# Optimization experiments

Hardware: AMD Instinct MI355X
Metric: run time of the kernel (lower is better)

## Reference

```python
import jax, jax.numpy as jnp
import numpy as np
import math

PS = 8          # patch_size
OUT_C = 16      # out_channels
D_MODEL = 64
P_STATE = 32
BANDLIMIT = 1.0
STEP_SCALE = 1.0  # dt1 reference rate


def _ln(x, g, b, eps=1e-5):
    mu = jnp.mean(x, -1, keepdims=True)
    var = jnp.mean((x - mu) ** 2, -1, keepdims=True)
    return (x - mu) * jax.lax.rsqrt(var + eps) * g + b


def _forward(x, W_embed, b_embed, g1, beta1, Lambda_re, Lambda_im, B_re, B_im,
             C_re, C_im, D, log_step, g2, beta2, W_enc, W_dec, g3, beta3, W_out, b_out):
    b, t, h, w = x.shape
    hp, wp = h // PS, w // PS
    n = hp * wp
    # patchify: [b,t,h,w] -> [b,t,n,ps*ps]
    xp = x.reshape(b, t, hp, PS, wp, PS).transpose(0, 1, 2, 4, 3, 5).reshape(b, t, n, PS * PS)
    xe = xp @ W_embed.T + b_embed                              # [b,t,n,d]
    u = xe.transpose(0, 2, 1, 3).reshape(b * n, t, D_MODEL)    # [(b n), t, d]

    # ---- S5Block: pre-norm -> diagonal SSM -> gelu + residual -> GEGLU FFN ----
    fx = _ln(u, g1, beta1)
    Lam = Lambda_re + 1j * Lambda_im                           # [P] complex eigenvalues
    step = STEP_SCALE * jnp.exp(log_step)                      # [P]
    Lbar = jnp.exp(Lam * step)                                 # ZOH: A_bar
    Bbar = ((Lbar - 1.0) / Lam)[:, None] * (B_re + 1j * B_im)  # ZOH: B_bar [P,d]
    # bandlimit mask on C (freqs = step*|Im(Lambda)|/(2pi) < bandlimit/2)
    freqs = step * jnp.abs(Lambda_im) / (2.0 * math.pi)
    mask = (freqs < BANDLIMIT * 0.5).astype(C_re.dtype)
    Cc = (C_re + 1j * C_im) * mask[None, :]                    # [d,P]

    Bu = jnp.einsum('ntd,pd->ntp', fx.astype(jnp.complex64), Bbar)   # [(bn),t,P]
    A = jnp.broadcast_to(Lbar.astype(jnp.complex64), (1, t, P_STATE))

    def comb(e1, e2):
        a1, b1 = e1
        a2, b2 = e2
        return a1 * a2, a2 * b1 + b2

    _, xs = jax.lax.associative_scan(comb, (A, Bu), axis=1)    # x_k = A*x_{k-1} + Bu_k (x_0 = 0)
    ys = jnp.einsum('ntp,dp->ntd', xs, Cc).real + fx * D       # y = Re(C x) + D u
    xb = jax.nn.gelu(ys, approximate=False) + fx

    fx2 = _ln(xb, g2, beta2)
    enc = fx2 @ W_enc.T                                        # [(bn),t,2d]
    a, gate = jnp.split(enc, 2, axis=-1)
    xb = (a * jax.nn.gelu(gate, approximate=False)) @ W_dec.T + fx2

    # ---- take last timestep, project, unpatchify ----
    x_last = xb[:, -1, :]                                      # [(bn), d]
    proj = _ln(x_last, g3, beta3) @ W_out.T + b_out            # [(bn), C*ps*ps]
    y = proj.reshape(b, hp, wp, OUT_C, PS, PS).transpose(0, 3, 1, 4, 2, 5).reshape(b, OUT_C, h, w)
    return y


def setup_inputs() -> dict:
    key = jax.random.key(0)
    ks = jax.random.split(key, 12)
    d, P, pp = D_MODEL, P_STATE, PS * PS
    return dict(
        x=jax.random.normal(ks[0], (8, 15, 480, 640), jnp.float32),
        W_embed=jax.random.normal(ks[1], (d, pp), jnp.float32) / math.sqrt(pp),
        b_embed=jnp.zeros((d,), jnp.float32),
        g1=jnp.ones((d,), jnp.float32), beta1=jnp.zeros((d,), jnp.float32),
        Lambda_re=-0.5 * jnp.ones((P,), jnp.float32),
        Lambda_im=math.pi * (1.0 + jnp.arange(P, dtype=jnp.float32)),
        B_re=jax.random.normal(ks[2], (P, d), jnp.float32) / math.sqrt(d),
        B_im=jax.random.normal(ks[3], (P, d), jnp.float32) / math.sqrt(d),
        C_re=jax.random.normal(ks[4], (d, P), jnp.float32) / math.sqrt(P),
        C_im=jax.random.normal(ks[5], (d, P), jnp.float32) / math.sqrt(P),
        D=jax.random.normal(ks[6], (d,), jnp.float32),
        log_step=jax.random.uniform(ks[7], (P,), jnp.float32, math.log(1e-3), math.log(1e-1)),
        g2=jnp.ones((d,), jnp.float32), beta2=jnp.zeros((d,), jnp.float32),
        W_enc=jax.random.normal(ks[8], (2 * d, d), jnp.float32) / math.sqrt(d),
        W_dec=jax.random.normal(ks[9], (d, d), jnp.float32) / math.sqrt(d),
        g3=jnp.ones((d,), jnp.float32), beta3=jnp.zeros((d,), jnp.float32),
        W_out=jax.random.normal(ks[10], (OUT_C * pp, d), jnp.float32) / math.sqrt(d),
        b_out=jnp.zeros((OUT_C * pp,), jnp.float32),
    )


def reference(x, W_embed, b_embed, g1, beta1, Lambda_re, Lambda_im, B_re, B_im,
              C_re, C_im, D, log_step, g2, beta2, W_enc, W_dec, g3, beta3, W_out, b_out):
    return _forward(x, W_embed, b_embed, g1, beta1, Lambda_re, Lambda_im, B_re, B_im,
                    C_re, C_im, D, log_step, g2, beta2, W_enc, W_dec, g3, beta3, W_out, b_out)
```

## Files before the change

kernel.cpp:

```cpp
#include <hip/hip_runtime.h>
#include <math.h>


typedef __attribute__((ext_vector_type(8))) short short8;
typedef __attribute__((ext_vector_type(4))) float f32x4;

#define MFMA16(a, b, c) __builtin_amdgcn_mfma_f32_16x16x32_bf16((a), (b), (c), 0, 0, 0)

__device__ __forceinline__ short f2bf(float f) {
  union { float f; unsigned u; } v; v.f = f;
  unsigned r = (v.u + 0x7fffu + ((v.u >> 16) & 1u)) >> 16;
  return (short)r;
}
__device__ __forceinline__ float geluf(float x) {
  return 0.5f * x * (1.0f + erff(x * 0.70710678118654752f));
}
__device__ __forceinline__ short8 packfrag(const f32x4& a, const f32x4& b) {
  short8 o;
  o[0] = f2bf(a[0]); o[1] = f2bf(a[1]); o[2] = f2bf(a[2]); o[3] = f2bf(a[3]);
  o[4] = f2bf(b[0]); o[5] = f2bf(b[1]); o[6] = f2bf(b[2]); o[7] = f2bf(b[3]);
  return o;
}
__device__ __forceinline__ int ecmap(int i, int m) {
  return (i >> 1) * 32 + (m >> 2) * 8 + (i & 1) * 4 + (m & 3);
}
__device__ __forceinline__ void bbar_factors(const float* Lre, const float* Lim,
                                             const float* lstep, int p,
                                             float& fre, float& fim) {
  float st = expf(lstep[p]);
  float lr = Lre[p], li = Lim[p];
  float er = expf(lr * st);
  float lbr = er * cosf(li * st), lbi = er * sinf(li * st);
  float u = lbr - 1.0f, v = lbi;
  float den = lr * lr + li * li;
  fre = (u * lr + v * li) / den;
  fim = (v * lr - u * li) / den;
}

__global__ __launch_bounds__(256) void k0_prep(
    const float* __restrict__ W_embed, const float* __restrict__ g1,
    const float* __restrict__ be1, const float* __restrict__ Lre,
    const float* __restrict__ Lim, const float* __restrict__ Bre,
    const float* __restrict__ Bim, const float* __restrict__ Cre,
    const float* __restrict__ Cim, const float* __restrict__ lstep,
    const float* __restrict__ W_enc, const float* __restrict__ W_dec,
    const float* __restrict__ W_out, short* __restrict__ wimg,
    float* __restrict__ bu0) {
  const int bid = blockIdx.x;
  if (bid == 44) {
    int q = threadIdx.x;
    if (q < 64) {
      int c = q >> 5, p = q & 31;
      float fre, fim; bbar_factors(Lre, Lim, lstep, p, fre, fim);
      float s = 0.f;
      for (int d = 0; d < 64; ++d) {
        float br = Bre[p * 64 + d], bi = Bim[p * 64 + d];
        float val = c ? (fre * bi + fim * br) : (fre * br - fim * bi);
        s += be1[d] * val;
      }
      bu0[q] = s;
    }
    return;
  }
  const int w = threadIdx.x >> 6, lane = threadIdx.x & 63;
  const int m = lane & 15, qd = lane >> 4;
  const int f = bid * 4 + w;
  short v[8];
  if (f < 8) {
    int i = f >> 1, kt = f & 1, chan = ecmap(i, m), k0 = kt * 32 + qd * 8;
#pragma unroll
    for (int j = 0; j < 8; ++j) v[j] = f2bf(W_embed[chan * 64 + k0 + j]);
  } else if (f < 16) {
    int fi = f - 8, i = fi >> 1, kt = fi & 1;
    int comp = i & 1, p = (i >> 1) * 16 + m, d0 = kt * 32 + qd * 8;
    float fre, fim; bbar_factors(Lre, Lim, lstep, p, fre, fim);
#pragma unroll
    for (int j = 0; j < 8; ++j) {
      int d = d0 + j;
      float br = Bre[p * 64 + d], bi = Bim[p * 64 + d];
      float val = comp ? (fre * bi + fim * br) : (fre * br - fim * bi);
      v[j] = f2bf(g1[d] * val);
    }
  } else if (f < 24) {
    int fi = f - 16, i = fi >> 1, kt = fi & 1, chan = ecmap(i, m);
#pragma unroll
    for (int j = 0; j < 8; ++j) {
      int comp = j >> 2, p = kt * 16 + qd * 4 + (j & 3);
      float stp = expf(lstep[p]);
      float fr = stp * fabsf(Lim[p]) * (1.0f / 6.28318530717958648f);
      float msk = (fr < 0.5f) ? 1.f : 0.f;
      float val = comp ? -Cim[chan * 32 + p] * msk : Cre[chan * 32 + p] * msk;
      v[j] = f2bf(val);
    }
  } else if (f < 40) {
    int fi = f - 24, i = fi >> 1, kt = fi & 1;
    int row = (i < 4) ? ecmap(i, m) : 64 + ecmap(i - 4, m);
#pragma unroll
    for (int j = 0; j < 8; ++j) v[j] = f2bf(W_enc[row * 64 + kt * 32 + qd * 8 + j]);
  } else if (f < 48) {
    int fi = f - 40, i = fi >> 1, kt = fi & 1, row = ecmap(i, m);
#pragma unroll
    for (int j = 0; j < 8; ++j) v[j] = f2bf(W_dec[row * 64 + kt * 32 + qd * 8 + j]);
  } else {
    int fi = f - 48, i = fi >> 1, kt = fi & 1, row = i * 16 + m;
#pragma unroll
    for (int j = 0; j < 8; ++j) v[j] = f2bf(W_out[row * 64 + kt * 32 + qd * 8 + j]);
  }
  short8 sv;
#pragma unroll
  for (int j = 0; j < 8; ++j) sv[j] = v[j];
  *(short8*)&wimg[(f * 64 + lane) * 8] = sv;
}

__global__ __launch_bounds__(320) void k1_fused(
    const float* __restrict__ x, const short* __restrict__ wimg_g,
    const float* __restrict__ bu0_g, const float* __restrict__ Lre,
    const float* __restrict__ Lim, const float* __restrict__ lstep,
    const float* __restrict__ g1, const float* __restrict__ be1,
    const float* __restrict__ bemb, const float* __restrict__ Dv,
    const float* __restrict__ g2, const float* __restrict__ be2,
    const float* __restrict__ g3, const float* __restrict__ be3,
    const float* __restrict__ b_out, float* __restrict__ y) {
  __shared__ __align__(16) char smem[57344];
#define WF(id) (*(const short8*)(smem + (id) * 1024 + lane * 16))

  const int tid = threadIdx.x;
  const int wv = tid >> 6, lane = tid & 63;
  const int s = lane & 15, qd = lane >> 4;

  int cb[4];
  f32x4 bec[4], bu0c[4];
#pragma unroll
  for (int nt = 0; nt < 4; ++nt) {
    cb[nt] = (nt >> 1) * 32 + qd * 8 + (nt & 1) * 4;
    bec[nt] = *(const f32x4*)(bemb + cb[nt]);
    bu0c[nt] = *(const f32x4*)(bu0_g + (nt & 1) * 32 + (nt >> 1) * 16 + qd * 4);
  }
  f32x4 lbr[2], lbi[2];
#pragma unroll
  for (int k = 0; k < 2; ++k)
#pragma unroll
    for (int r = 0; r < 4; ++r) {
      int p = k * 16 + qd * 4 + r;
      float st = expf(lstep[p]);
      float er = expf(Lre[p] * st);
      lbr[k][r] = er * cosf(Lim[p] * st);
      lbi[k][r] = er * sinf(Lim[p] * st);
    }

  const int b_i = blockIdx.x / 60;
  const int ph = blockIdx.x % 60;
  const int tb0 = ((b_i * 15) * 480 + ph * 8) * 640;
  const int sbase = blockIdx.x * 80 + wv * 16;
  int rb[4];
#pragma unroll
  for (int kt = 0; kt < 2; ++kt)
#pragma unroll
    for (int h = 0; h < 2; ++h)
      rb[kt * 2 + h] = (kt * 4 + qd) * 2560 + (wv * 16 + s) * 32 + h * 16;

#define STAGE(bufofs, tt)                                                     \
  {                                                                           \
    const float* gsrc = x + tb0 + (tt) * 307200 + wv * 1024;                  \
    char* lb = smem + (bufofs) + wv * 4096;                                   \
    _Pragma("unroll") for (int j = 0; j < 4; ++j)                             \
        __builtin_amdgcn_global_load_lds(                                     \
            (const __attribute__((address_space(1))) void*)(gsrc + j * 256 +  \
                                                            lane * 4),        \
            (__attribute__((address_space(3))) void*)(lb + j * 1024),         \
            16, 0, 0);                                                        \
  }

  STAGE(16384, 0);
  STAGE(36864, 1);
  {
    float4* wdst = (float4*)smem;
    const float4* wsrc = (const float4*)wimg_g;
    for (int i = tid; i < 1024; i += 320) wdst[i] = wsrc[i];
  }
  asm volatile("s_waitcnt vmcnt(0) lgkmcnt(0)" ::: "memory");
  __builtin_amdgcn_s_barrier();

  const f32x4 zf = {0.f, 0.f, 0.f, 0.f};
  f32x4 state[4] = {zf, zf, zf, zf};
  f32x4 xh[4];

  for (int t = 0; t < 15; ++t) {
    const char* bufr = smem + 16384 + (t & 1) * 20480;
    f32x4 vcur[4];
#pragma unroll
    for (int q = 0; q < 4; ++q) vcur[q] = *(const f32x4*)(bufr + rb[q]);
    asm volatile("s_waitcnt lgkmcnt(0)" ::: "memory");
    __builtin_amdgcn_s_barrier();
    if (t < 13) STAGE(16384 + (t & 1) * 20480, t + 2);

    short8 pa0 = packfrag(vcur[0], vcur[1]);
    short8 pa1 = packfrag(vcur[2], vcur[3]);
    f32x4 c1[4];
#pragma unroll
    for (int i = 0; i < 4; ++i) {
      f32x4 acc = MFMA16(WF(i * 2), pa0, zf);
      acc = MFMA16(WF(i * 2 + 1), pa1, acc);
      c1[i] = acc + bec[i];
    }
    float sm = 0.f, sq = 0.f;
#pragma unroll
    for (int nt = 0; nt < 4; ++nt)
#pragma unroll
      for (int i = 0; i < 4; ++i) { sm += c1[nt][i]; sq += c1[nt][i] * c1[nt][i]; }
    sm += __shfl_xor(sm, 16); sq += __shfl_xor(sq, 16);
    sm += __shfl_xor(sm, 32); sq += __shfl_xor(sq, 32);
    float mean = sm * 0.015625f;
    float rstd = rsqrtf(sq * 0.015625f - mean * mean + 1e-5f);
#pragma unroll
    for (int nt = 0; nt < 4; ++nt) xh[nt] = (c1[nt] - mean) * rstd;
    short8 xa0 = packfrag(xh[0], xh[1]);
    short8 xa1 = packfrag(xh[2], xh[3]);
#pragma unroll
    for (int k = 0; k < 2; ++k) {
      f32x4 re = state[2 * k], im = state[2 * k + 1];
      state[2 * k]     = lbr[k] * re - lbi[k] * im + bu0c[2 * k];
      state[2 * k + 1] = lbr[k] * im + lbi[k] * re + bu0c[2 * k + 1];
    }
#pragma unroll
    for (int i = 0; i < 4; ++i) {
      state[i] = MFMA16(WF(8 + i * 2), xa0, state[i]);
      state[i] = MFMA16(WF(8 + i * 2 + 1), xa1, state[i]);
    }

    if (t < 14) {
      if (t < 13) asm volatile("s_waitcnt vmcnt(4)" ::: "memory");
      else        asm volatile("s_waitcnt vmcnt(0)" ::: "memory");
      __builtin_amdgcn_s_barrier();
    }
  }
#undef STAGE

  __syncthreads();
  {
    float4* dst = (float4*)(smem + 16384);
    const float4* src = (const float4*)(wimg_g + 16 * 512);
    for (int i = tid; i < 2048; i += 320) dst[i] = src[i];
  }
  __syncthreads();

  f32x4 g1c[4], b1c[4], Dc[4], g2c[4], b2c[4];
#pragma unroll
  for (int nt = 0; nt < 4; ++nt) {
    g1c[nt] = *(const f32x4*)(g1 + cb[nt]);
    b1c[nt] = *(const f32x4*)(be1 + cb[nt]);
    Dc[nt] = *(const f32x4*)(Dv + cb[nt]);
    g2c[nt] = *(const f32x4*)(g2 + cb[nt]);
    b2c[nt] = *(const f32x4*)(be2 + cb[nt]);
  }
  f32x4 fxl[4];
#pragma unroll
  for (int nt = 0; nt < 4; ++nt) fxl[nt] = xh[nt] * g1c[nt] + b1c[nt];

  short8 xsa0 = packfrag(state[0], state[1]);
  short8 xsa1 = packfrag(state[2], state[3]);
  f32x4 xbv[4];
#pragma unroll
  for (int i = 0; i < 4; ++i) {
    f32x4 acc = fxl[i] * Dc[i];
    acc = MFMA16(WF(16 + i * 2), xsa0, acc);
    acc = MFMA16(WF(16 + i * 2 + 1), xsa1, acc);
#pragma unroll
    for (int r = 0; r < 4; ++r) xbv[i][r] = geluf(acc[r]) + fxl[i][r];
  }
  float sm2 = 0.f, sq2 = 0.f;
#pragma unroll
  for (int nt = 0; nt < 4; ++nt)
#pragma unroll
    for (int i = 0; i < 4; ++i) { sm2 += xbv[nt][i]; sq2 += xbv[nt][i] * xbv[nt][i]; }
  sm2 += __shfl_xor(sm2, 16); sq2 += __shfl_xor(sq2, 16);
  sm2 += __shfl_xor(sm2, 32); sq2 += __shfl_xor(sq2, 32);
  float mean2 = sm2 * 0.015625f;
  float rstd2 = rsqrtf(sq2 * 0.015625f - mean2 * mean2 + 1e-5f);
  f32x4 fx2[4];
#pragma unroll
  for (int nt = 0; nt < 4; ++nt)
    fx2[nt] = (xbv[nt] - mean2) * rstd2 * g2c[nt] + b2c[nt];

  short8 fa0 = packfrag(fx2[0], fx2[1]);
  short8 fa1 = packfrag(fx2[2], fx2[3]);
  f32x4 e[8];
#pragma unroll
  for (int i = 0; i < 8; ++i) {
    f32x4 acc = MFMA16(WF(24 + i * 2), fa0, zf);
    e[i] = MFMA16(WF(24 + i * 2 + 1), fa1, acc);
  }
  f32x4 hv[4];
#pragma unroll
  for (int nt = 0; nt < 4; ++nt)
#pragma unroll
    for (int i = 0; i < 4; ++i) hv[nt][i] = e[nt][i] * geluf(e[nt + 4][i]);

  short8 ha0 = packfrag(hv[0], hv[1]);
  short8 ha1 = packfrag(hv[2], hv[3]);
  f32x4 xo[4];
#pragma unroll
  for (int i = 0; i < 4; ++i) {
    f32x4 acc = fx2[i];
    acc = MFMA16(WF(40 + i * 2), ha0, acc);
    xo[i] = MFMA16(WF(40 + i * 2 + 1), ha1, acc);
  }

  float sm3 = 0.f, sq3 = 0.f;
#pragma unroll
  for (int nt = 0; nt < 4; ++nt)
#pragma unroll
    for (int i = 0; i < 4; ++i) { sm3 += xo[nt][i]; sq3 += xo[nt][i] * xo[nt][i]; }
  sm3 += __shfl_xor(sm3, 16); sq3 += __shfl_xor(sq3, 16);
  sm3 += __shfl_xor(sm3, 32); sq3 += __shfl_xor(sq3, 32);
  float mean3 = sm3 * 0.015625f;
  float rstd3 = rsqrtf(sq3 * 0.015625f - mean3 * mean3 + 1e-5f);
  f32x4 z[4];
#pragma unroll
  for (int nt = 0; nt < 4; ++nt) {
    f32x4 g3c = *(const f32x4*)(g3 + cb[nt]);
    f32x4 b3c = *(const f32x4*)(be3 + cb[nt]);
    z[nt] = (xo[nt] - mean3) * rstd3 * g3c + b3c;
  }
  short8 za = packfrag(z[0], z[1]);
  short8 zb = packfrag(z[2], z[3]);

  const int seq = sbase + s;
  const int bi2 = seq / 4800, prr = seq % 4800;
  const int phh = prr / 80, pww = prr % 80;
  const int obase = (bi2 * 16 * 480 + phh * 8) * 640 + pww * 8;
  const short* wob = wimg_g + 48 * 512;

#pragma unroll 4
  for (int ntg = 0; ntg < 64; ++ntg) {
    short8 a0 = *(const short8*)&wob[(ntg * 2 + 0) * 512 + lane * 8];
    short8 a1 = *(const short8*)&wob[(ntg * 2 + 1) * 512 + lane * 8];
    int o0 = ntg * 16 + qd * 4;
    f32x4 acc = *(const f32x4*)(b_out + o0);
    acc = MFMA16(a0, za, acc);
    acc = MFMA16(a1, zb, acc);
    int c = o0 >> 6, pi = (o0 >> 3) & 7, pj = o0 & 7;
    *(f32x4*)&y[obase + c * 307200 + pi * 640 + pj] = acc;
  }
#undef WF
}

extern "C" void kernel_launch(void* const* d_in, const int* in_sizes, int n_in,
                              void* d_out, int out_size, void* d_ws, size_t ws_size,
                              hipStream_t stream) {
  const float* x       = (const float*)d_in[0];
  const float* W_embed = (const float*)d_in[1];
  const float* b_embed = (const float*)d_in[2];
  const float* g1      = (const float*)d_in[3];
  const float* beta1   = (const float*)d_in[4];
  const float* Lre     = (const float*)d_in[5];
  const float* Lim     = (const float*)d_in[6];
  const float* Bre     = (const float*)d_in[7];
  const float* Bim     = (const float*)d_in[8];
  const float* Cre     = (const float*)d_in[9];
  const float* Cim     = (const float*)d_in[10];
  const float* Dv      = (const float*)d_in[11];
  const float* lstep   = (const float*)d_in[12];
  const float* g2      = (const float*)d_in[13];
  const float* beta2   = (const float*)d_in[14];
  const float* W_enc   = (const float*)d_in[15];
  const float* W_dec   = (const float*)d_in[16];
  const float* g3      = (const float*)d_in[17];
  const float* beta3   = (const float*)d_in[18];
  const float* W_out   = (const float*)d_in[19];
  const float* b_out   = (const float*)d_in[20];
  float* y = (float*)d_out;

  short* wimg = (short*)d_ws;
  float* bu0 = (float*)((char*)d_ws + 176 * 1024);

  k0_prep<<<dim3(45), dim3(256), 0, stream>>>(W_embed, g1, beta1, Lre, Lim,
                                              Bre, Bim, Cre, Cim, lstep,
                                              W_enc, W_dec, W_out, wimg, bu0);
  k1_fused<<<dim3(480), dim3(320), 0, stream>>>(x, wimg, bu0, Lre, Lim, lstep,
                                                g1, beta1, b_embed, Dv, g2,
                                                beta2, g3, beta3, b_out, y);
}
```

Measured before the change: 338.6 us.

## Replace LDS-staged input pipeline with direct register prefetch and drop shared memory

Removes the shared-memory double-buffered global_load_lds staging of x and the LDS copies of weight fragments. Each wave now loads its input rows straight into registers with a three-deep rotating prefetch, keeps the first 16 weight fragments in registers, and reads the rest from global or cache. Blocks shrink from 5 to 4 waves and the grid grows from 480 to 600. This drops barriers and LDS traffic and allows higher occupancy, at the cost of more registers and less coalesced global loads.

```diff
diff --git a/kernel.cpp b/kernel.cpp
--- a/kernel.cpp
+++ b/kernel.cpp
@@ -112,7 +112,53 @@
   *(short8*)&wimg[(f * 64 + lane) * 8] = sv;
 }
 
-__global__ __launch_bounds__(320) void k1_fused(
+
+#define LOADX(X, T)                                                           \
+  {                                                                           \
+    const float* rp_ = xbase + (T) * 307200;                                  \
+    X[0] = *(const f32x4*)rp_;                                                \
+    X[1] = *(const f32x4*)(rp_ + 4);                                          \
+    X[2] = *(const f32x4*)(rp_ + 2560);                                       \
+    X[3] = *(const f32x4*)(rp_ + 2564);                                       \
+  }
+
+#define BODY(X, T)                                                            \
+  {                                                                           \
+    short8 pa0 = packfrag(X[0], X[1]);                                        \
+    short8 pa1 = packfrag(X[2], X[3]);                                        \
+    if ((T) + 3 < 15) LOADX(X, (T) + 3);                                      \
+    f32x4 c1[4];                                                              \
+    _Pragma("unroll") for (int i = 0; i < 4; ++i) {                           \
+      f32x4 acc = MFMA16(we[i * 2], pa0, zf);                                 \
+      acc = MFMA16(we[i * 2 + 1], pa1, acc);                                  \
+      c1[i] = acc + bec[i];                                                   \
+    }                                                                         \
+    float sm = 0.f, sq = 0.f;                                                 \
+    _Pragma("unroll") for (int nt = 0; nt < 4; ++nt)                          \
+        _Pragma("unroll") for (int i = 0; i < 4; ++i) {                       \
+      sm += c1[nt][i];                                                        \
+      sq += c1[nt][i] * c1[nt][i];                                            \
+    }                                                                         \
+    sm += __shfl_xor(sm, 16); sq += __shfl_xor(sq, 16);                       \
+    sm += __shfl_xor(sm, 32); sq += __shfl_xor(sq, 32);                       \
+    float mean = sm * 0.015625f;                                              \
+    float rstd = rsqrtf(sq * 0.015625f - mean * mean + 1e-5f);                \
+    _Pragma("unroll") for (int nt = 0; nt < 4; ++nt)                          \
+        xh[nt] = (c1[nt] - mean) * rstd;                                      \
+    short8 xa0 = packfrag(xh[0], xh[1]);                                      \
+    short8 xa1 = packfrag(xh[2], xh[3]);                                      \
+    _Pragma("unroll") for (int k = 0; k < 2; ++k) {                           \
+      f32x4 re = state[2 * k], im = state[2 * k + 1];                         \
+      state[2 * k]     = lbr[k] * re - lbi[k] * im + bu0c[2 * k];             \
+      state[2 * k + 1] = lbr[k] * im + lbi[k] * re + bu0c[2 * k + 1];         \
+    }                                                                         \
+    _Pragma("unroll") for (int i = 0; i < 4; ++i) {                           \
+      state[i] = MFMA16(we[8 + i * 2], xa0, state[i]);                        \
+      state[i] = MFMA16(we[8 + i * 2 + 1], xa1, state[i]);                    \
+    }                                                                         \
+  }
+
+__global__ __launch_bounds__(256) void k1_fused(
     const float* __restrict__ x, const short* __restrict__ wimg_g,
     const float* __restrict__ bu0_g, const float* __restrict__ Lre,
     const float* __restrict__ Lim, const float* __restrict__ lstep,
@@ -121,12 +167,15 @@
     const float* __restrict__ g2, const float* __restrict__ be2,
     const float* __restrict__ g3, const float* __restrict__ be3,
     const float* __restrict__ b_out, float* __restrict__ y) {
-  __shared__ __align__(16) char smem[57344];
-#define WF(id) (*(const short8*)(smem + (id) * 1024 + lane * 16))
+#define GW(id) (*(const short8*)&wimg_g[(id) * 512 + lane * 8])
 
   const int tid = threadIdx.x;
   const int wv = tid >> 6, lane = tid & 63;
   const int s = lane & 15, qd = lane >> 4;
+
+  short8 we[16];
+#pragma unroll
+  for (int i = 0; i < 16; ++i) we[i] = GW(i);
 
   int cb[4];
   f32x4 bec[4], bu0c[4];
@@ -148,101 +197,28 @@
       lbi[k][r] = er * sinf(Lim[p] * st);
     }
 
-  const int b_i = blockIdx.x / 60;
-  const int ph = blockIdx.x % 60;
-  const int tb0 = ((b_i * 15) * 480 + ph * 8) * 640;
-  const int sbase = blockIdx.x * 80 + wv * 16;
-  int rb[4];
-#pragma unroll
-  for (int kt = 0; kt < 2; ++kt)
-#pragma unroll
-    for (int h = 0; h < 2; ++h)
-      rb[kt * 2 + h] = (kt * 4 + qd) * 2560 + (wv * 16 + s) * 32 + h * 16;
-
-#define STAGE(bufofs, tt)                                                     \
-  {                                                                           \
-    const float* gsrc = x + tb0 + (tt) * 307200 + wv * 1024;                  \
-    char* lb = smem + (bufofs) + wv * 4096;                                   \
-    _Pragma("unroll") for (int j = 0; j < 4; ++j)                             \
-        __builtin_amdgcn_global_load_lds(                                     \
-            (const __attribute__((address_space(1))) void*)(gsrc + j * 256 +  \
-                                                            lane * 4),        \
-            (__attribute__((address_space(3))) void*)(lb + j * 1024),         \
-            16, 0, 0);                                                        \
-  }
-
-  STAGE(16384, 0);
-  STAGE(36864, 1);
-  {
-    float4* wdst = (float4*)smem;
-    const float4* wsrc = (const float4*)wimg_g;
-    for (int i = tid; i < 1024; i += 320) wdst[i] = wsrc[i];
-  }
-  asm volatile("s_waitcnt vmcnt(0) lgkmcnt(0)" ::: "memory");
-  __builtin_amdgcn_s_barrier();
+  const int sbase = (blockIdx.x * 4 + wv) * 16;
+  const int b_i = sbase / 4800;
+  const int pr = sbase % 4800;
+  const int ph = pr / 80;
+  const int pw0 = pr % 80;
+  const float* xbase = x + ((b_i * 15) * 480 + ph * 8 + qd) * 640 + (pw0 + s) * 8;
 
   const f32x4 zf = {0.f, 0.f, 0.f, 0.f};
   f32x4 state[4] = {zf, zf, zf, zf};
   f32x4 xh[4];
 
-  for (int t = 0; t < 15; ++t) {
-    const char* bufr = smem + 16384 + (t & 1) * 20480;
-    f32x4 vcur[4];
-#pragma unroll
-    for (int q = 0; q < 4; ++q) vcur[q] = *(const f32x4*)(bufr + rb[q]);
-    asm volatile("s_waitcnt lgkmcnt(0)" ::: "memory");
-    __builtin_amdgcn_s_barrier();
-    if (t < 13) STAGE(16384 + (t & 1) * 20480, t + 2);
-
-    short8 pa0 = packfrag(vcur[0], vcur[1]);
-    short8 pa1 = packfrag(vcur[2], vcur[3]);
-    f32x4 c1[4];
-#pragma unroll
-    for (int i = 0; i < 4; ++i) {
-      f32x4 acc = MFMA16(WF(i * 2), pa0, zf);
-      acc = MFMA16(WF(i * 2 + 1), pa1, acc);
-      c1[i] = acc + bec[i];
-    }
-    float sm = 0.f, sq = 0.f;
-#pragma unroll
-    for (int nt = 0; nt < 4; ++nt)
-#pragma unroll
-      for (int i = 0; i < 4; ++i) { sm += c1[nt][i]; sq += c1[nt][i] * c1[nt][i]; }
-    sm += __shfl_xor(sm, 16); sq += __shfl_xor(sq, 16);
-    sm += __shfl_xor(sm, 32); sq += __shfl_xor(sq, 32);
-    float mean = sm * 0.015625f;
-    float rstd = rsqrtf(sq * 0.015625f - mean * mean + 1e-5f);
-#pragma unroll
-    for (int nt = 0; nt < 4; ++nt) xh[nt] = (c1[nt] - mean) * rstd;
-    short8 xa0 = packfrag(xh[0], xh[1]);
-    short8 xa1 = packfrag(xh[2], xh[3]);
-#pragma unroll
-    for (int k = 0; k < 2; ++k) {
-      f32x4 re = state[2 * k], im = state[2 * k + 1];
-      state[2 * k]     = lbr[k] * re - lbi[k] * im + bu0c[2 * k];
-      state[2 * k + 1] = lbr[k] * im + lbi[k] * re + bu0c[2 * k + 1];
-    }
-#pragma unroll
-    for (int i = 0; i < 4; ++i) {
-      state[i] = MFMA16(WF(8 + i * 2), xa0, state[i]);
-      state[i] = MFMA16(WF(8 + i * 2 + 1), xa1, state[i]);
-    }
-
-    if (t < 14) {
-      if (t < 13) asm volatile("s_waitcnt vmcnt(4)" ::: "memory");
-      else        asm volatile("s_waitcnt vmcnt(0)" ::: "memory");
-      __builtin_amdgcn_s_barrier();
-    }
-  }
-#undef STAGE
-
-  __syncthreads();
-  {
-    float4* dst = (float4*)(smem + 16384);
-    const float4* src = (const float4*)(wimg_g + 16 * 512);
-    for (int i = tid; i < 2048; i += 320) dst[i] = src[i];
-  }
-  __syncthreads();
+  f32x4 xsA[4], xsB[4], xsC[4];
+  LOADX(xsA, 0);
+  LOADX(xsB, 1);
+  LOADX(xsC, 2);
+
+  for (int tt = 0; tt < 5; ++tt) {
+    const int t0 = tt * 3;
+    BODY(xsA, t0 + 0);
+    BODY(xsB, t0 + 1);
+    BODY(xsC, t0 + 2);
+  }
 
   f32x4 g1c[4], b1c[4], Dc[4], g2c[4], b2c[4];
 #pragma unroll
@@ -263,8 +239,8 @@
 #pragma unroll
   for (int i = 0; i < 4; ++i) {
     f32x4 acc = fxl[i] * Dc[i];
-    acc = MFMA16(WF(16 + i * 2), xsa0, acc);
-    acc = MFMA16(WF(16 + i * 2 + 1), xsa1, acc);
+    acc = MFMA16(GW(16 + i * 2), xsa0, acc);
+    acc = MFMA16(GW(16 + i * 2 + 1), xsa1, acc);
 #pragma unroll
     for (int r = 0; r < 4; ++r) xbv[i][r] = geluf(acc[r]) + fxl[i][r];
   }
@@ -287,8 +263,8 @@
   f32x4 e[8];
 #pragma unroll
   for (int i = 0; i < 8; ++i) {
-    f32x4 acc = MFMA16(WF(24 + i * 2), fa0, zf);
-    e[i] = MFMA16(WF(24 + i * 2 + 1), fa1, acc);
+    f32x4 acc = MFMA16(GW(24 + i * 2), fa0, zf);
+    e[i] = MFMA16(GW(24 + i * 2 + 1), fa1, acc);
   }
   f32x4 hv[4];
 #pragma unroll
@@ -302,8 +278,8 @@
 #pragma unroll
   for (int i = 0; i < 4; ++i) {
     f32x4 acc = fx2[i];
-    acc = MFMA16(WF(40 + i * 2), ha0, acc);
-    xo[i] = MFMA16(WF(40 + i * 2 + 1), ha1, acc);
+    acc = MFMA16(GW(40 + i * 2), ha0, acc);
+    xo[i] = MFMA16(GW(40 + i * 2 + 1), ha1, acc);
   }
 
   float sm3 = 0.f, sq3 = 0.f;
@@ -342,7 +318,7 @@
     int c = o0 >> 6, pi = (o0 >> 3) & 7, pj = o0 & 7;
     *(f32x4*)&y[obase + c * 307200 + pi * 640 + pj] = acc;
   }
-#undef WF
+#undef GW
 }
 
 extern "C" void kernel_launch(void* const* d_in, const int* in_sizes, int n_in,
@@ -377,7 +353,7 @@
   k0_prep<<<dim3(45), dim3(256), 0, stream>>>(W_embed, g1, beta1, Lre, Lim,
                                               Bre, Bim, Cre, Cim, lstep,
                                               W_enc, W_dec, W_out, wimg, bu0);
-  k1_fused<<<dim3(480), dim3(320), 0, stream>>>(x, wimg, bu0, Lre, Lim, lstep,
+  k1_fused<<<dim3(600), dim3(256), 0, stream>>>(x, wimg, bu0, Lre, Lim, lstep,
                                                 g1, beta1, b_embed, Dv, g2,
                                                 beta2, g3, beta3, b_out, y);
 }
```

After: 358.3 us. 1.06x slower.
